# Kernel tuning notes

Measured on AMD Instinct MI355X. Metric: run time of the kernel, lower is better.

Reference implementation:

```python
import jax, jax.numpy as jnp
import numpy as np

N_WIRES = 4
DEPTH = 2
N_PATCH = 196  # 14*14 2x2 patches of a 28x28 image


def _ry(state, theta, w):
    """Apply RY(theta) on wire w. state: [B,P,2,2,2,2]; theta: scalar or [B,P]."""
    ax = 2 + w
    half = theta * 0.5
    c = jnp.cos(half)
    s = jnp.sin(half)
    # broadcast angle over remaining wire axes
    c = c.reshape(c.shape + (1,) * (state.ndim - 1 - c.ndim))
    s = s.reshape(s.shape + (1,) * (state.ndim - 1 - s.ndim))
    s0 = jnp.take(state, 0, axis=ax)
    s1 = jnp.take(state, 1, axis=ax)
    return jnp.stack([c * s0 - s * s1, s * s0 + c * s1], axis=ax)


def _cnot(state, cw, tw):
    """CNOT with control wire cw, target wire tw."""
    ca, ta = 2 + cw, 2 + tw
    c0 = jnp.take(state, 0, axis=ca)
    c1 = jnp.take(state, 1, axis=ca)
    ta_adj = ta - 1 if ta > ca else ta  # axis shift after take along ca
    return jnp.stack([c0, jnp.flip(c1, axis=ta_adj)], axis=ca)


def _quanv_features(x, var_angles):
    """Batched exact 4-qubit state-vector sim over all 196 patches at once."""
    B = x.shape[0]
    img = x.reshape(B, 28, 28)
    # [B,14,2,14,2] -> [B,14,14,2,2] -> [B,196,4]: (r,c),(r,c+1),(r+1,c),(r+1,c+1)
    patches = img.reshape(B, 14, 2, 14, 2).transpose(0, 1, 3, 2, 4).reshape(B, N_PATCH, 4)
    # RY/CNOT circuit keeps amplitudes real -> real fp32 state [B,P,2,2,2,2]
    state = jnp.zeros((B, N_PATCH, 2, 2, 2, 2), dtype=x.dtype)
    state = state.at[:, :, 0, 0, 0, 0].set(1.0)
    # encoder: RY(pixel) on each wire
    for w in range(N_WIRES):
        state = _ry(state, patches[:, :, w], w)
    # variational layer: per depth, learnable RY on each wire + CNOT ring
    for d in range(DEPTH):
        for w in range(N_WIRES):
            state = _ry(state, var_angles[d, w], w)
        for cw in range(N_WIRES):
            state = _cnot(state, cw, (cw + 1) % N_WIRES)
    probs = state * state
    # <Z_w> = P(wire w = 0) - P(wire w = 1)
    feats = jnp.stack(
        [(jnp.take(probs, 0, axis=2 + w) - jnp.take(probs, 1, axis=2 + w)).sum(axis=(2, 3, 4))
         for w in range(N_WIRES)], axis=-1)  # [B,196,4]
    return feats.reshape(B, N_PATCH * N_WIRES)  # [B,784]


def setup_inputs() -> dict:
    key = jax.random.key(0)
    k1, k2, k3, k4 = jax.random.split(key, 4)
    B = 4096
    x = jax.random.uniform(k1, (B, 1, 28, 28), dtype=jnp.float32)  # pixel-like angles
    var_angles = jax.random.normal(k2, (DEPTH, N_WIRES), dtype=jnp.float32)
    W1 = jax.random.normal(k3, (256, 784), dtype=jnp.float32) * (1.0 / np.sqrt(784.0))
    b1 = jnp.zeros((256,), dtype=jnp.float32)
    W2 = jax.random.normal(k4, (10, 256), dtype=jnp.float32) * (1.0 / np.sqrt(256.0))
    b2 = jnp.zeros((10,), dtype=jnp.float32)
    return {"x": x, "var_angles": var_angles, "W1": W1, "b1": b1, "W2": W2, "b2": b2}


def reference(x, var_angles, W1, b1, W2, b2):
    feats = _quanv_features(x, var_angles)            # [B,784]
    h = jax.nn.relu(feats @ W1.T + b1)                # dropout is identity in eval
    logits = h @ W2.T + b2                            # [B,10]
    return jax.nn.log_softmax(logits, axis=-1)
```

## Files before the change

kernel.cpp:

```cpp
#include <hip/hip_runtime.h>
#include <math.h>

typedef short bf16x8 __attribute__((ext_vector_type(8)));
typedef float f32x4 __attribute__((ext_vector_type(4)));

__device__ __forceinline__ unsigned short f2bf(float f) {
    unsigned int u = __float_as_uint(f);
    u = (u + 0x7FFFu + ((u >> 16) & 1u)) >> 16;
    return (unsigned short)u;
}


__device__ __forceinline__ void ry_gate(float a[16], int bitpos, float c, float s) {
    const int mask = 1 << bitpos;
#pragma unroll
    for (int i = 0; i < 16; ++i) {
        if (!(i & mask)) {
            const int j = i | mask;
            const float a0 = a[i], a1 = a[j];
            a[i] = c * a0 - s * a1;
            a[j] = s * a0 + c * a1;
        }
    }
}

__device__ __forceinline__ void cnot_gate(float a[16], int cbit, int tbit) {
    const int cmask = 1 << cbit, tmask = 1 << tbit;
#pragma unroll
    for (int i = 0; i < 16; ++i) {
        if ((i & cmask) && !(i & tmask)) {
            const int j = i | tmask;
            const float tmp = a[i];
            a[i] = a[j];
            a[j] = tmp;
        }
    }
}

__global__ __launch_bounds__(256) void prep_quanv_kernel(
        const float* __restrict__ x, const float* __restrict__ var_angles,
        const float* __restrict__ W1,
        unsigned short* __restrict__ fhi, unsigned short* __restrict__ w1hi,
        int quanv_total) {
    const int blk = blockIdx.x;
    if (blk < 800) {
        const int id = blk * 256 + threadIdx.x;
        const int r = id / 800;
        const int c = id - r * 800;
        const float v = (c < 784) ? W1[r * 784 + c] : 0.f;
        w1hi[id] = f2bf(v);
        return;
    }

    const int idx = (blk - 800) * 256 + threadIdx.x;
    if (idx >= quanv_total) return;
    const int b = idx / 196;
    const int p = idx - b * 196;
    const int pr = p / 14;
    const int pc = p - pr * 14;

    const float* img = x + (size_t)b * 784;
    const float2 top = *(const float2*)(img + (2 * pr) * 28 + 2 * pc);
    const float2 bot = *(const float2*)(img + (2 * pr + 1) * 28 + 2 * pc);
    const float theta[4] = {top.x, top.y, bot.x, bot.y};

    float c[4], s[4];
#pragma unroll
    for (int w = 0; w < 4; ++w) {
        const float h = 0.5f * theta[w];
        s[w] = __sinf(h);
        c[w] = __cosf(h);
    }

    float a[16];
#pragma unroll
    for (int i = 0; i < 16; ++i) {
        float v = (i & 8) ? s[0] : c[0];
        v *= (i & 4) ? s[1] : c[1];
        v *= (i & 2) ? s[2] : c[2];
        v *= (i & 1) ? s[3] : c[3];
        a[i] = v;
    }

#pragma unroll
    for (int d = 0; d < 2; ++d) {
#pragma unroll
        for (int w = 0; w < 4; ++w) {
            const float h = 0.5f * var_angles[d * 4 + w];
            ry_gate(a, 3 - w, __cosf(h), __sinf(h));
        }
        cnot_gate(a, 3, 2);
        cnot_gate(a, 2, 1);
        cnot_gate(a, 1, 0);
        cnot_gate(a, 0, 3);
    }

    float z[4] = {0.f, 0.f, 0.f, 0.f};
#pragma unroll
    for (int i = 0; i < 16; ++i) {
        const float pr2 = a[i] * a[i];
        z[0] += (i & 8) ? -pr2 : pr2;
        z[1] += (i & 4) ? -pr2 : pr2;
        z[2] += (i & 2) ? -pr2 : pr2;
        z[3] += (i & 1) ? -pr2 : pr2;
    }

    ushort4 hv;
    unsigned short* hp = (unsigned short*)&hv;
#pragma unroll
    for (int w = 0; w < 4; ++w) hp[w] = f2bf(z[w]);
    *(ushort4*)(fhi + (size_t)b * 800 + p * 4) = hv;

    if (p < 4) {
        const ushort4 zz = {0, 0, 0, 0};
        *(ushort4*)(fhi + (size_t)b * 800 + 784 + p * 4) = zz;
    }
}

__global__ __launch_bounds__(256) void gemm1_mfma_kernel(
        const unsigned short* __restrict__ A_g, const unsigned short* __restrict__ B_g,
        const float* __restrict__ b1, float* __restrict__ H) {
    __shared__ unsigned short As[32][40];
    __shared__ unsigned short Bs[64][40];

    const int t = threadIdx.x;
    const int row0 = blockIdx.x * 32;
    const int col0 = blockIdx.y * 64;
    const int lane = t & 63;
    const int wv = t >> 6;
    const int q = lane >> 4;
    const int lm = lane & 15;
    const int mh = wv & 1;
    const int np = wv >> 1;

    const int sr = t >> 2;
    const int sk = (t & 3) * 8;

    const unsigned short* pB = B_g + (size_t)(col0 + sr) * 800 + sk;
    const unsigned short* pA = A_g + (size_t)(row0 + sr) * 800 + sk;

    f32x4 acc0 = (f32x4)(0.f), acc1 = (f32x4)(0.f);

    float4 vb = *(const float4*)pB;
    float4 va;
    if (t < 128) va = *(const float4*)pA;

    for (int k0 = 0; k0 < 800; k0 += 32) {
        __syncthreads();
        *(float4*)&Bs[sr][sk] = vb;
        if (t < 128) *(float4*)&As[sr][sk] = va;
        __syncthreads();

        if (k0 + 32 < 800) {
            vb = *(const float4*)(pB + k0 + 32);
            if (t < 128) va = *(const float4*)(pA + k0 + 32);
        }

        const bf16x8 a  = *(const bf16x8*)&As[mh * 16 + lm][q * 8];
        const bf16x8 b0 = *(const bf16x8*)&Bs[np * 32 + lm][q * 8];
        const bf16x8 b1v = *(const bf16x8*)&Bs[np * 32 + 16 + lm][q * 8];
        acc0 = __builtin_amdgcn_mfma_f32_16x16x32_bf16(a, b0, acc0, 0, 0, 0);
        acc1 = __builtin_amdgcn_mfma_f32_16x16x32_bf16(a, b1v, acc1, 0, 0, 0);
    }

    const int n0 = col0 + np * 32 + lm;
    const float bias0 = b1[n0];
    const float bias1 = b1[n0 + 16];
#pragma unroll
    for (int i = 0; i < 4; ++i) {
        const int m = row0 + mh * 16 + q * 4 + i;
        H[(size_t)m * 256 + n0]      = fmaxf(acc0[i] + bias0, 0.f);
        H[(size_t)m * 256 + n0 + 16] = fmaxf(acc1[i] + bias1, 0.f);
    }
}

__global__ __launch_bounds__(256) void mlp2_lsm_kernel(
        const float* __restrict__ H, const float* __restrict__ W2,
        const float* __restrict__ b2, float* __restrict__ out) {
    const int lane = threadIdx.x & 63;
    const int wv = threadIdx.x >> 6;
    const int b = blockIdx.x * 4 + wv;

    const float4 h = *(const float4*)(H + (size_t)b * 256 + lane * 4);

    float logits[10];
#pragma unroll
    for (int j = 0; j < 10; ++j) {
        const float4 w = *(const float4*)(W2 + (size_t)j * 256 + lane * 4);
        float d = h.x * w.x + h.y * w.y + h.z * w.z + h.w * w.w;
#pragma unroll
        for (int off = 32; off > 0; off >>= 1) d += __shfl_xor(d, off, 64);
        logits[j] = d + b2[j];
    }

    float m = logits[0];
#pragma unroll
    for (int j = 1; j < 10; ++j) m = fmaxf(m, logits[j]);
    float se = 0.f;
#pragma unroll
    for (int j = 0; j < 10; ++j) se += expf(logits[j] - m);
    const float lse = m + logf(se);

    if (lane == 0) {
#pragma unroll
        for (int j = 0; j < 10; ++j) out[(size_t)b * 10 + j] = logits[j] - lse;
    }
}


extern "C" void kernel_launch(void* const* d_in, const int* in_sizes, int n_in,
                              void* d_out, int out_size, void* d_ws, size_t ws_size,
                              hipStream_t stream) {
    const float* x   = (const float*)d_in[0];
    const float* var = (const float*)d_in[1];
    const float* W1  = (const float*)d_in[2];
    const float* b1  = (const float*)d_in[3];
    const float* W2  = (const float*)d_in[4];
    const float* b2  = (const float*)d_in[5];
    float* out = (float*)d_out;

    const int B = in_sizes[0] / 784;
    const int KP = 800;

    char* ws = (char*)d_ws;
    unsigned short* fhi  = (unsigned short*)ws;
    unsigned short* w1hi = fhi + (size_t)B * KP;
    float* H = (float*)(w1hi + (size_t)256 * KP);

    const int quanv_total = B * 196;
    const int quanv_blocks = (quanv_total + 255) / 256;
    prep_quanv_kernel<<<800 + quanv_blocks, 256, 0, stream>>>(
        x, var, W1, fhi, w1hi, quanv_total);
    gemm1_mfma_kernel<<<dim3(B / 32, 256 / 64), 256, 0, stream>>>(fhi, w1hi, b1, H);
    mlp2_lsm_kernel<<<B / 4, 256, 0, stream>>>(H, W2, b2, out);
}
```

Before: 97.79 us.

## Fuse quanv simulation, first GEMM, and output layer into one kernel

Replaces the three-kernel pipeline (quanv prep, GEMM1, MLP2+log-softmax) with a W1 bf16 conversion kernel plus one fused kernel. Each 512-thread block computes the bf16 features for 16 images directly into shared memory, runs the MFMA GEMM against W1 streamed from global memory with register double-buffering, writes ReLU activations to shared memory, and finishes the second layer and log-softmax there. This removes the global round trips for the feature matrix and hidden activations and two launches. In exchange, only 256 blocks run, and each block rereads all of W1 from global or L2 memory. The cosines and sines of the variational angles are also hoisted out of the per-patch loop.

```diff
diff --git a/kernel.cpp b/kernel.cpp
--- a/kernel.cpp
+++ b/kernel.cpp
@@ -3,11 +3,23 @@
 
 typedef short bf16x8 __attribute__((ext_vector_type(8)));
 typedef float f32x4 __attribute__((ext_vector_type(4)));
+
+#define KP 800
+#define AS_LD 808
+#define HS_LD 260
 
 __device__ __forceinline__ unsigned short f2bf(float f) {
     unsigned int u = __float_as_uint(f);
     u = (u + 0x7FFFu + ((u >> 16) & 1u)) >> 16;
     return (unsigned short)u;
+}
+
+__global__ __launch_bounds__(256) void w1cvt_kernel(
+        const float* __restrict__ W1, unsigned short* __restrict__ w1bf) {
+    const int id = blockIdx.x * 256 + threadIdx.x;
+    const int r = id / KP;
+    const int c = id - r * KP;
+    w1bf[id] = f2bf((c < 784) ? W1[r * 784 + c] : 0.f);
 }
 
 
@@ -37,174 +49,166 @@
     }
 }
 
-__global__ __launch_bounds__(256) void prep_quanv_kernel(
+__global__ __launch_bounds__(512) void fused_kernel(
         const float* __restrict__ x, const float* __restrict__ var_angles,
-        const float* __restrict__ W1,
-        unsigned short* __restrict__ fhi, unsigned short* __restrict__ w1hi,
-        int quanv_total) {
-    const int blk = blockIdx.x;
-    if (blk < 800) {
-        const int id = blk * 256 + threadIdx.x;
-        const int r = id / 800;
-        const int c = id - r * 800;
-        const float v = (c < 784) ? W1[r * 784 + c] : 0.f;
-        w1hi[id] = f2bf(v);
-        return;
-    }
-
-    const int idx = (blk - 800) * 256 + threadIdx.x;
-    if (idx >= quanv_total) return;
-    const int b = idx / 196;
-    const int p = idx - b * 196;
-    const int pr = p / 14;
-    const int pc = p - pr * 14;
-
-    const float* img = x + (size_t)b * 784;
-    const float2 top = *(const float2*)(img + (2 * pr) * 28 + 2 * pc);
-    const float2 bot = *(const float2*)(img + (2 * pr + 1) * 28 + 2 * pc);
-    const float theta[4] = {top.x, top.y, bot.x, bot.y};
-
-    float c[4], s[4];
-#pragma unroll
-    for (int w = 0; w < 4; ++w) {
-        const float h = 0.5f * theta[w];
-        s[w] = __sinf(h);
-        c[w] = __cosf(h);
-    }
-
-    float a[16];
-#pragma unroll
-    for (int i = 0; i < 16; ++i) {
-        float v = (i & 8) ? s[0] : c[0];
-        v *= (i & 4) ? s[1] : c[1];
-        v *= (i & 2) ? s[2] : c[2];
-        v *= (i & 1) ? s[3] : c[3];
-        a[i] = v;
-    }
-
-#pragma unroll
-    for (int d = 0; d < 2; ++d) {
+        const unsigned short* __restrict__ w1bf, const float* __restrict__ b1,
+        const float* __restrict__ W2, const float* __restrict__ b2,
+        float* __restrict__ out) {
+    __shared__ unsigned short As[16][AS_LD];
+    __shared__ float Hs[16][HS_LD];
+    __shared__ float W2s[2560];
+    __shared__ float b1s[256];
+    __shared__ float b2s[12];
+
+    const int tid = threadIdx.x;
+    const int r0 = blockIdx.x * 16;
+
+#pragma unroll
+    for (int i = tid; i < 2560; i += 512) W2s[i] = W2[i];
+    if (tid < 256) b1s[tid] = b1[tid];
+    if (tid < 10) b2s[tid] = b2[tid];
+
+    if (tid < 64) {
+        const ushort4 zz = {0, 0, 0, 0};
+        *(ushort4*)&As[tid >> 2][784 + (tid & 3) * 4] = zz;
+    }
+
+    float vvc[8], vvs[8];
+#pragma unroll
+    for (int i = 0; i < 8; ++i) {
+        const float h = 0.5f * var_angles[i];
+        vvs[i] = __sinf(h);
+        vvc[i] = __cosf(h);
+    }
+
+    for (int i = tid; i < 16 * 196; i += 512) {
+        const int lr = i / 196;
+        const int p = i - lr * 196;
+        const int pr = p / 14;
+        const int pc = p - pr * 14;
+
+        const float* img = x + (size_t)(r0 + lr) * 784;
+        const float2 top = *(const float2*)(img + (2 * pr) * 28 + 2 * pc);
+        const float2 bot = *(const float2*)(img + (2 * pr + 1) * 28 + 2 * pc);
+        const float theta[4] = {top.x, top.y, bot.x, bot.y};
+
+        float c[4], s[4];
 #pragma unroll
         for (int w = 0; w < 4; ++w) {
-            const float h = 0.5f * var_angles[d * 4 + w];
-            ry_gate(a, 3 - w, __cosf(h), __sinf(h));
-        }
-        cnot_gate(a, 3, 2);
-        cnot_gate(a, 2, 1);
-        cnot_gate(a, 1, 0);
-        cnot_gate(a, 0, 3);
-    }
-
-    float z[4] = {0.f, 0.f, 0.f, 0.f};
-#pragma unroll
-    for (int i = 0; i < 16; ++i) {
-        const float pr2 = a[i] * a[i];
-        z[0] += (i & 8) ? -pr2 : pr2;
-        z[1] += (i & 4) ? -pr2 : pr2;
-        z[2] += (i & 2) ? -pr2 : pr2;
-        z[3] += (i & 1) ? -pr2 : pr2;
-    }
-
-    ushort4 hv;
-    unsigned short* hp = (unsigned short*)&hv;
-#pragma unroll
-    for (int w = 0; w < 4; ++w) hp[w] = f2bf(z[w]);
-    *(ushort4*)(fhi + (size_t)b * 800 + p * 4) = hv;
-
-    if (p < 4) {
-        const ushort4 zz = {0, 0, 0, 0};
-        *(ushort4*)(fhi + (size_t)b * 800 + 784 + p * 4) = zz;
-    }
-}
-
-__global__ __launch_bounds__(256) void gemm1_mfma_kernel(
-        const unsigned short* __restrict__ A_g, const unsigned short* __restrict__ B_g,
-        const float* __restrict__ b1, float* __restrict__ H) {
-    __shared__ unsigned short As[32][40];
-    __shared__ unsigned short Bs[64][40];
-
-    const int t = threadIdx.x;
-    const int row0 = blockIdx.x * 32;
-    const int col0 = blockIdx.y * 64;
-    const int lane = t & 63;
-    const int wv = t >> 6;
+            const float h = 0.5f * theta[w];
+            s[w] = __sinf(h);
+            c[w] = __cosf(h);
+        }
+
+        float a[16];
+#pragma unroll
+        for (int k = 0; k < 16; ++k) {
+            float v = (k & 8) ? s[0] : c[0];
+            v *= (k & 4) ? s[1] : c[1];
+            v *= (k & 2) ? s[2] : c[2];
+            v *= (k & 1) ? s[3] : c[3];
+            a[k] = v;
+        }
+
+#pragma unroll
+        for (int d = 0; d < 2; ++d) {
+#pragma unroll
+            for (int w = 0; w < 4; ++w)
+                ry_gate(a, 3 - w, vvc[d * 4 + w], vvs[d * 4 + w]);
+            cnot_gate(a, 3, 2);
+            cnot_gate(a, 2, 1);
+            cnot_gate(a, 1, 0);
+            cnot_gate(a, 0, 3);
+        }
+
+        float z[4] = {0.f, 0.f, 0.f, 0.f};
+#pragma unroll
+        for (int k = 0; k < 16; ++k) {
+            const float pr2 = a[k] * a[k];
+            z[0] += (k & 8) ? -pr2 : pr2;
+            z[1] += (k & 4) ? -pr2 : pr2;
+            z[2] += (k & 2) ? -pr2 : pr2;
+            z[3] += (k & 1) ? -pr2 : pr2;
+        }
+
+        ushort4 hv;
+        unsigned short* hp = (unsigned short*)&hv;
+#pragma unroll
+        for (int w = 0; w < 4; ++w) hp[w] = f2bf(z[w]);
+        *(ushort4*)&As[lr][p * 4] = hv;
+    }
+    __syncthreads();
+
+    const int lane = tid & 63;
+    const int wv = tid >> 6;
     const int q = lane >> 4;
     const int lm = lane & 15;
-    const int mh = wv & 1;
-    const int np = wv >> 1;
-
-    const int sr = t >> 2;
-    const int sk = (t & 3) * 8;
-
-    const unsigned short* pB = B_g + (size_t)(col0 + sr) * 800 + sk;
-    const unsigned short* pA = A_g + (size_t)(row0 + sr) * 800 + sk;
+    const int n0 = wv * 32;
+
+    const unsigned short* pB0 = w1bf + (size_t)(n0 + lm) * KP + q * 8;
+    const unsigned short* pB1 = pB0 + (size_t)16 * KP;
 
     f32x4 acc0 = (f32x4)(0.f), acc1 = (f32x4)(0.f);
 
-    float4 vb = *(const float4*)pB;
-    float4 va;
-    if (t < 128) va = *(const float4*)pA;
-
-    for (int k0 = 0; k0 < 800; k0 += 32) {
-        __syncthreads();
-        *(float4*)&Bs[sr][sk] = vb;
-        if (t < 128) *(float4*)&As[sr][sk] = va;
-        __syncthreads();
-
-        if (k0 + 32 < 800) {
-            vb = *(const float4*)(pB + k0 + 32);
-            if (t < 128) va = *(const float4*)(pA + k0 + 32);
-        }
-
-        const bf16x8 a  = *(const bf16x8*)&As[mh * 16 + lm][q * 8];
-        const bf16x8 b0 = *(const bf16x8*)&Bs[np * 32 + lm][q * 8];
-        const bf16x8 b1v = *(const bf16x8*)&Bs[np * 32 + 16 + lm][q * 8];
-        acc0 = __builtin_amdgcn_mfma_f32_16x16x32_bf16(a, b0, acc0, 0, 0, 0);
-        acc1 = __builtin_amdgcn_mfma_f32_16x16x32_bf16(a, b1v, acc1, 0, 0, 0);
-    }
-
-    const int n0 = col0 + np * 32 + lm;
-    const float bias0 = b1[n0];
-    const float bias1 = b1[n0 + 16];
+    bf16x8 b0a = *(const bf16x8*)(pB0);
+    bf16x8 b1a = *(const bf16x8*)(pB1);
+    bf16x8 b0b = *(const bf16x8*)(pB0 + 32);
+    bf16x8 b1b = *(const bf16x8*)(pB1 + 32);
+
+    for (int k0 = 0; k0 < KP; k0 += 32) {
+        const bf16x8 a = *(const bf16x8*)&As[lm][k0 + q * 8];
+        acc0 = __builtin_amdgcn_mfma_f32_16x16x32_bf16(a, b0a, acc0, 0, 0, 0);
+        acc1 = __builtin_amdgcn_mfma_f32_16x16x32_bf16(a, b1a, acc1, 0, 0, 0);
+        b0a = b0b;
+        b1a = b1b;
+        if (k0 + 64 < KP) {
+            b0b = *(const bf16x8*)(pB0 + k0 + 64);
+            b1b = *(const bf16x8*)(pB1 + k0 + 64);
+        }
+    }
+
+    const float bias0 = b1s[n0 + lm];
+    const float bias1 = b1s[n0 + 16 + lm];
 #pragma unroll
     for (int i = 0; i < 4; ++i) {
-        const int m = row0 + mh * 16 + q * 4 + i;
-        H[(size_t)m * 256 + n0]      = fmaxf(acc0[i] + bias0, 0.f);
-        H[(size_t)m * 256 + n0 + 16] = fmaxf(acc1[i] + bias1, 0.f);
-    }
-}
-
-__global__ __launch_bounds__(256) void mlp2_lsm_kernel(
-        const float* __restrict__ H, const float* __restrict__ W2,
-        const float* __restrict__ b2, float* __restrict__ out) {
-    const int lane = threadIdx.x & 63;
-    const int wv = threadIdx.x >> 6;
-    const int b = blockIdx.x * 4 + wv;
-
-    const float4 h = *(const float4*)(H + (size_t)b * 256 + lane * 4);
-
-    float logits[10];
+        const int r = q * 4 + i;
+        Hs[r][n0 + lm]      = fmaxf(acc0[i] + bias0, 0.f);
+        Hs[r][n0 + 16 + lm] = fmaxf(acc1[i] + bias1, 0.f);
+    }
+    __syncthreads();
+
+    const int er = tid >> 5;
+    const int el = tid & 31;
+
+    const float4 h0 = *(const float4*)&Hs[er][el * 8];
+    const float4 h1 = *(const float4*)&Hs[er][el * 8 + 4];
+
+    float part[10];
 #pragma unroll
     for (int j = 0; j < 10; ++j) {
-        const float4 w = *(const float4*)(W2 + (size_t)j * 256 + lane * 4);
-        float d = h.x * w.x + h.y * w.y + h.z * w.z + h.w * w.w;
-#pragma unroll
-        for (int off = 32; off > 0; off >>= 1) d += __shfl_xor(d, off, 64);
-        logits[j] = d + b2[j];
-    }
-
-    float m = logits[0];
-#pragma unroll
-    for (int j = 1; j < 10; ++j) m = fmaxf(m, logits[j]);
+        const float4 w0 = *(const float4*)&W2s[j * 256 + el * 8];
+        const float4 w1 = *(const float4*)&W2s[j * 256 + el * 8 + 4];
+        part[j] = h0.x * w0.x + h0.y * w0.y + h0.z * w0.z + h0.w * w0.w +
+                  h1.x * w1.x + h1.y * w1.y + h1.z * w1.z + h1.w * w1.w;
+    }
+#pragma unroll
+    for (int mask = 1; mask < 32; mask <<= 1) {
+#pragma unroll
+        for (int j = 0; j < 10; ++j) part[j] += __shfl_xor(part[j], mask, 64);
+    }
+
+    float lg[10];
+#pragma unroll
+    for (int j = 0; j < 10; ++j) lg[j] = part[j] + b2s[j];
+    float m = lg[0];
+#pragma unroll
+    for (int j = 1; j < 10; ++j) m = fmaxf(m, lg[j]);
     float se = 0.f;
 #pragma unroll
-    for (int j = 0; j < 10; ++j) se += expf(logits[j] - m);
+    for (int j = 0; j < 10; ++j) se += expf(lg[j] - m);
     const float lse = m + logf(se);
 
-    if (lane == 0) {
-#pragma unroll
-        for (int j = 0; j < 10; ++j) out[(size_t)b * 10 + j] = logits[j] - lse;
-    }
+    if (el < 10) out[(size_t)(r0 + er) * 10 + el] = lg[el] - lse;
 }
 
 
@@ -220,17 +224,9 @@
     float* out = (float*)d_out;
 
     const int B = in_sizes[0] / 784;
-    const int KP = 800;
-
-    char* ws = (char*)d_ws;
-    unsigned short* fhi  = (unsigned short*)ws;
-    unsigned short* w1hi = fhi + (size_t)B * KP;
-    float* H = (float*)(w1hi + (size_t)256 * KP);
-
-    const int quanv_total = B * 196;
-    const int quanv_blocks = (quanv_total + 255) / 256;
-    prep_quanv_kernel<<<800 + quanv_blocks, 256, 0, stream>>>(
-        x, var, W1, fhi, w1hi, quanv_total);
-    gemm1_mfma_kernel<<<dim3(B / 32, 256 / 64), 256, 0, stream>>>(fhi, w1hi, b1, H);
-    mlp2_lsm_kernel<<<B / 4, 256, 0, stream>>>(H, W2, b2, out);
-}
+
+    unsigned short* w1bf = (unsigned short*)d_ws;
+
+    w1cvt_kernel<<<(256 * KP) / 256, 256, 0, stream>>>(W1, w1bf);
+    fused_kernel<<<B / 16, 512, 0, stream>>>(x, var, w1bf, b1, W2, b2, out);
+}
```

Result: faster. 89.71 us (-8.3%).
